# Kernel tuning notes

Measured on AMD Instinct MI355X. Metric: run time of the kernel, lower is better.

## Reference

```python
import jax, jax.numpy as jnp
import numpy as np

NEG = -1e9
CLIP = 10.0  # tanh clipping constant for SingleHeadAttention logits


def layer_norm(x, g, b, eps=1e-5):
    mu = jnp.mean(x, axis=-1, keepdims=True)
    var = jnp.var(x, axis=-1, keepdims=True)
    return (x - mu) * jax.lax.rsqrt(var + eps) * g + b


def setup_inputs() -> dict:
    key = jax.random.key(0)
    ks = jax.random.split(key, 16)
    B, A, N, E, Hf = 4096, 16, 128, 128, 128
    s = 0.02
    inp = {
        "agent_embed": jax.random.normal(ks[0], (B, A, E), jnp.float32),
        "city_embed": jax.random.normal(ks[1], (B, N, E), jnp.float32),
        "acts": jax.random.randint(ks[2], (B, A), 0, N, jnp.int32),
        # cross-attention layer params
        "Wq": jax.random.normal(ks[3], (E, E), jnp.float32) * s,
        "Wk": jax.random.normal(ks[4], (E, E), jnp.float32) * s,
        "Wv": jax.random.normal(ks[5], (E, E), jnp.float32) * s,
        "Wo": jax.random.normal(ks[6], (E, E), jnp.float32) * s,
        "ln1_g": jnp.ones((E,), jnp.float32),
        "ln1_b": jnp.zeros((E,), jnp.float32),
        "W1": jax.random.normal(ks[7], (E, Hf), jnp.float32) * s,
        "b1": jnp.zeros((Hf,), jnp.float32),
        "W2": jax.random.normal(ks[8], (Hf, E), jnp.float32) * s,
        "b2": jnp.zeros((E,), jnp.float32),
        "ln2_g": jnp.ones((E,), jnp.float32),
        "ln2_b": jnp.zeros((E,), jnp.float32),
        # single-head attention params
        "Wq_s": jax.random.normal(ks[9], (E, E), jnp.float32) * s,
        "Wk_s": jax.random.normal(ks[10], (E, E), jnp.float32) * s,
    }
    return inp


def reference(agent_embed, city_embed, acts, Wq, Wk, Wv, Wo, ln1_g, ln1_b,
              W1, b1, W2, b2, ln2_g, ln2_b, Wq_s, Wk_s):
    B, A, E = agent_embed.shape
    H = 8
    dh = E // H

    # ---- conflict mask construction ----
    eq = acts[:, :, None] == acts[:, None, :]            # [B,A,A] True = same city
    ident = jnp.eye(A, dtype=bool)[None]                 # [1,A,A]
    conflict = jnp.where(acts[:, :, None] == 0, ident, eq)
    mask = ~conflict                                     # True = blocked in attention

    # ---- gather per-agent selected city embeddings ----
    selected = jnp.take_along_axis(city_embed, acts[:, :, None].astype(jnp.int32), axis=1)  # [B,A,E]

    # ---- cross-attention layer (num_layers = 1) ----
    cac = selected
    q = (cac @ Wq).reshape(B, A, H, dh)
    k = (agent_embed @ Wk).reshape(B, A, H, dh)
    v = (agent_embed @ Wv).reshape(B, A, H, dh)
    scores = jnp.einsum("bqhd,bkhd->bhqk", q, k) / np.sqrt(dh).astype(np.float32)
    scores = jnp.where(mask[:, None, :, :], NEG, scores)
    attn = jax.nn.softmax(scores, axis=-1)
    out = jnp.einsum("bhqk,bkhd->bqhd", attn, v).reshape(B, A, E) @ Wo
    h = layer_norm(cac + out, ln1_g, ln1_b)
    ffn = jax.nn.relu(h @ W1 + b1) @ W2 + b2
    cac = layer_norm(h + ffn, ln2_g, ln2_b)

    # ---- single-head attention producing logits [B,A,A] ----
    qs = cac @ Wq_s
    ks_ = agent_embed @ Wk_s
    logits = jnp.einsum("bqe,bke->bqk", qs, ks_) / np.sqrt(E).astype(np.float32)
    logits = CLIP * jnp.tanh(logits)
    logits = jnp.where(mask, NEG, logits)
    return logits
```

## Files before the change

### kernel.cpp

```cpp
#include <hip/hip_runtime.h>
#include <hip/hip_bf16.h>
#include <math.h>

typedef __attribute__((ext_vector_type(8))) short bfrag;
typedef __attribute__((ext_vector_type(4))) short short4v;
typedef __attribute__((ext_vector_type(4))) float f32x4;

#define LDK 136

static __device__ __forceinline__ float b2f(short s)
{
    unsigned int u = ((unsigned int)(unsigned short)s) << 16;
    float f;
    __builtin_memcpy(&f, &u, 4);
    return f;
}

static __device__ __forceinline__ short4v pack4(f32x4 a)
{
    short4v o;
#pragma unroll
    for (int r = 0; r < 4; ++r) {
        __hip_bfloat16 h = __float2bfloat16(a[r]);
        short s;
        __builtin_memcpy(&s, &h, 2);
        o[r] = s;
    }
    return o;
}

static __device__ __forceinline__ bfrag pack8(f32x4 a, f32x4 b)
{
    bfrag o;
#pragma unroll
    for (int j = 0; j < 4; ++j) {
        __hip_bfloat16 h = __float2bfloat16(a[j]);
        short s;
        __builtin_memcpy(&s, &h, 2);
        o[j] = s;
    }
#pragma unroll
    for (int j = 0; j < 4; ++j) {
        __hip_bfloat16 h = __float2bfloat16(b[j]);
        short s;
        __builtin_memcpy(&s, &h, 2);
        o[4 + j] = s;
    }
    return o;
}

__global__ __launch_bounds__(256) void prep_weights(
    const float* __restrict__ Wq, const float* __restrict__ Wk,
    const float* __restrict__ Wv, const float* __restrict__ Wo,
    const float* __restrict__ W1, const float* __restrict__ W2,
    const float* __restrict__ Wqs, const float* __restrict__ Wks,
    __hip_bfloat16* __restrict__ out)
{
    __shared__ __hip_bfloat16 t[128 * 17];
    const float* Ws[8] = {Wq, Wk, Wv, Wo, W1, W2, Wqs, Wks};
    const int mat = blockIdx.x >> 3;
    const int slab = blockIdx.x & 7;
    const float* W = Ws[mat];
    const int n0 = slab * 16;

#pragma unroll
    for (int p = 0; p < 2; ++p) {
        int idx = p * 256 + threadIdx.x;
        int k = idx >> 2, c4 = idx & 3;
        float4 f = *(const float4*)(W + k * 128 + n0 + c4 * 4);
        __hip_bfloat16* d = t + k * 17 + c4 * 4;
        d[0] = __float2bfloat16(f.x); d[1] = __float2bfloat16(f.y);
        d[2] = __float2bfloat16(f.z); d[3] = __float2bfloat16(f.w);
    }
    __syncthreads();
    {
        int m = threadIdx.x >> 4;
        int idx = threadIdx.x & 15;
        int k0 = idx * 8;
        int kk = idx >> 2;
        int quad = idx & 3;
        __hip_bfloat16 v[8];
#pragma unroll
        for (int j = 0; j < 8; ++j) v[j] = t[(k0 + j) * 17 + m];
        __hip_bfloat16* o = out + (size_t)mat * 16384
                          + (size_t)(slab * 4 + kk) * 512 + (quad * 16 + m) * 8;
        *(bfrag*)o = *(const bfrag*)v;
    }
}

__device__ __forceinline__ void mmT8(const bfrag x[4],
                                     const __hip_bfloat16* sW,
                                     int lane, f32x4 acc[8])
{
    const f32x4 z = {0.f, 0.f, 0.f, 0.f};
#pragma unroll
    for (int ct = 0; ct < 8; ++ct) acc[ct] = z;
#pragma unroll
    for (int kk = 0; kk < 4; ++kk)
#pragma unroll
        for (int ct = 0; ct < 8; ++ct) {
            bfrag w = *(const bfrag*)(sW + (ct * 4 + kk) * 512 + lane * 8);
            acc[ct] = __builtin_amdgcn_mfma_f32_16x16x32_bf16(w, x[kk], acc[ct], 0, 0, 0);
        }
}

__device__ __forceinline__ void mmR8(const bfrag x[4],
                                     const __hip_bfloat16* sW,
                                     int lane, f32x4 acc[8])
{
    const f32x4 z = {0.f, 0.f, 0.f, 0.f};
#pragma unroll
    for (int ct = 0; ct < 8; ++ct) acc[ct] = z;
#pragma unroll
    for (int kk = 0; kk < 4; ++kk)
#pragma unroll
        for (int ct = 0; ct < 8; ++ct) {
            bfrag w = *(const bfrag*)(sW + (ct * 4 + kk) * 512 + lane * 8);
            acc[ct] = __builtin_amdgcn_mfma_f32_16x16x32_bf16(x[kk], w, acc[ct], 0, 0, 0);
        }
}

__global__ __launch_bounds__(256) void fused_model(
    const float* __restrict__ agent_embed,
    const float* __restrict__ city_embed,
    const int* __restrict__ acts,
    const __hip_bfloat16* __restrict__ wts,
    const float* __restrict__ ln1g, const float* __restrict__ ln1b,
    const float* __restrict__ b1, const float* __restrict__ b2,
    const float* __restrict__ ln2g, const float* __restrict__ ln2b,
    float* __restrict__ out)
{
    __shared__ __align__(16) __hip_bfloat16 sW[16384];
    __shared__ __align__(16) __hip_bfloat16 sbAll[4 * 16 * LDK];

    const int tid = threadIdx.x;
    const int wave = tid >> 6;
    const int lane = tid & 63;
    const int m = lane & 15;
    const int quad = lane >> 4;
    const int b = blockIdx.x * 4 + wave;
    __hip_bfloat16* const sb = sbAll + wave * (16 * LDK);

    bfrag wreg[8];

#define PRE(mat)                                                                \
    {                                                                           \
        const __hip_bfloat16* src = wts + (size_t)(mat) * 16384;                \
        _Pragma("unroll")                                                       \
        for (int i = 0; i < 8; ++i)                                             \
            wreg[i] = *(const bfrag*)(src + (i * 256 + tid) * 8);               \
    }
#define COMMIT()                                                                \
    {                                                                           \
        _Pragma("unroll")                                                       \
        for (int i = 0; i < 8; ++i)                                             \
            *(bfrag*)(sW + (i * 256 + tid) * 8) = wreg[i];                      \
    }

    const int aq = acts[b * 16 + m];
    bool keep[4];
#pragma unroll
    for (int r = 0; r < 4; ++r) {
        int ak = __shfl(aq, quad * 4 + r, 16);
        keep[r] = (aq == 0) ? (quad * 4 + r == m) : (ak == aq);
    }

    PRE(1);

    const float* arow = agent_embed + ((size_t)b * 16 + m) * 128;
    const float* crow = city_embed + ((size_t)b * 128 + aq) * 128;
    bfrag xa[4], xsk[4];
#pragma unroll
    for (int kk = 0; kk < 4; ++kk) {
        f32x4 a0 = *(const f32x4*)(arow + kk * 32 + quad * 8);
        f32x4 a1 = *(const f32x4*)(arow + kk * 32 + quad * 8 + 4);
        xa[kk] = pack8(a0, a1);
        f32x4 c0 = *(const f32x4*)(crow + kk * 32 + quad * 8);
        f32x4 c1 = *(const f32x4*)(crow + kk * 32 + quad * 8 + 4);
        xsk[kk] = pack8(c0, c1);
    }

    COMMIT();
    __syncthreads();

    f32x4 acc[8];
    short4v kf[8], vf[8], ksf[8], qf[8];

    PRE(2);
    mmT8(xa, sW, lane, acc);
#pragma unroll
    for (int ct = 0; ct < 8; ++ct) kf[ct] = pack4(acc[ct]);
    __syncthreads();
    COMMIT(); __syncthreads();

    PRE(7);
    mmR8(xa, sW, lane, acc);
#pragma unroll
    for (int ct = 0; ct < 8; ++ct) vf[ct] = pack4(acc[ct]);
    __syncthreads();
    COMMIT(); __syncthreads();

    PRE(0);
    mmT8(xa, sW, lane, acc);
#pragma unroll
    for (int ct = 0; ct < 8; ++ct) ksf[ct] = pack4(acc[ct]);
    __syncthreads();
    COMMIT(); __syncthreads();

    PRE(3);
    mmT8(xsk, sW, lane, acc);
#pragma unroll
    for (int ct = 0; ct < 8; ++ct) qf[ct] = pack4(acc[ct]);

    {
        const f32x4 z4 = {0.f, 0.f, 0.f, 0.f};
#pragma unroll
        for (int h = 0; h < 8; ++h) {
            f32x4 sc = __builtin_amdgcn_mfma_f32_16x16x16bf16_1k(kf[h], qf[h], z4, 0, 0, 0);
            float e[4], s = 0.f;
#pragma unroll
            for (int r = 0; r < 4; ++r) {
                e[r] = keep[r] ? __expf(sc[r] * 0.25f) : 0.f;
                s += e[r];
            }
            s += __shfl_xor(s, 16, 64);
            s += __shfl_xor(s, 32, 64);
            float inv = __builtin_amdgcn_rcpf(s);
            f32x4 p;
#pragma unroll
            for (int r = 0; r < 4; ++r) p[r] = e[r] * inv;
            short4v pa = pack4(p);
            f32x4 o4 = __builtin_amdgcn_mfma_f32_16x16x16bf16_1k(vf[h], pa, z4, 0, 0, 0);
            *(short4v*)(sb + m * LDK + h * 16 + quad * 4) = pack4(o4);
        }
    }
    bfrag xo[4];
#pragma unroll
    for (int kk = 0; kk < 4; ++kk)
        xo[kk] = *(const bfrag*)(sb + m * LDK + kk * 32 + quad * 8);
    __syncthreads();
    COMMIT(); __syncthreads();

    PRE(4);
    mmT8(xo, sW, lane, acc);
#pragma unroll
    for (int ct = 0; ct < 8; ++ct) {
        f32x4 cres = *(const f32x4*)(crow + ct * 16 + quad * 4);
#pragma unroll
        for (int r = 0; r < 4; ++r) acc[ct][r] += cres[r];
    }

    short4v hf[8];
    {
        float s = 0.f, s2 = 0.f;
#pragma unroll
        for (int ct = 0; ct < 8; ++ct)
#pragma unroll
            for (int r = 0; r < 4; ++r) { float v = acc[ct][r]; s += v; s2 += v * v; }
        s += __shfl_xor(s, 16, 64);  s += __shfl_xor(s, 32, 64);
        s2 += __shfl_xor(s2, 16, 64); s2 += __shfl_xor(s2, 32, 64);
        float mu = s * (1.f / 128.f);
        float var = s2 * (1.f / 128.f) - mu * mu;
        float rs = rsqrtf(var + 1e-5f);
#pragma unroll
        for (int ct = 0; ct < 8; ++ct) {
            f32x4 g4 = *(const f32x4*)(ln1g + ct * 16 + quad * 4);
            f32x4 bb4 = *(const f32x4*)(ln1b + ct * 16 + quad * 4);
            f32x4 hh;
#pragma unroll
            for (int r = 0; r < 4; ++r) hh[r] = (acc[ct][r] - mu) * rs * g4[r] + bb4[r];
            hf[ct] = pack4(hh);
            *(short4v*)(sb + m * LDK + ct * 16 + quad * 4) = hf[ct];
        }
    }
    bfrag hx[4];
#pragma unroll
    for (int kk = 0; kk < 4; ++kk)
        hx[kk] = *(const bfrag*)(sb + m * LDK + kk * 32 + quad * 8);
    __syncthreads();
    COMMIT(); __syncthreads();

    PRE(5);
    mmT8(hx, sW, lane, acc);
#pragma unroll
    for (int ct = 0; ct < 8; ++ct) {
        f32x4 bb4 = *(const f32x4*)(b1 + ct * 16 + quad * 4);
        f32x4 f;
#pragma unroll
        for (int r = 0; r < 4; ++r) f[r] = fmaxf(acc[ct][r] + bb4[r], 0.f);
        *(short4v*)(sb + m * LDK + ct * 16 + quad * 4) = pack4(f);
    }
    bfrag fx[4];
#pragma unroll
    for (int kk = 0; kk < 4; ++kk)
        fx[kk] = *(const bfrag*)(sb + m * LDK + kk * 32 + quad * 8);
    __syncthreads();
    COMMIT(); __syncthreads();

    PRE(6);
    mmT8(fx, sW, lane, acc);
#pragma unroll
    for (int ct = 0; ct < 8; ++ct) {
        f32x4 bb4 = *(const f32x4*)(b2 + ct * 16 + quad * 4);
#pragma unroll
        for (int r = 0; r < 4; ++r) acc[ct][r] += bb4[r] + b2f(hf[ct][r]);
    }

    {
        float s = 0.f, s2 = 0.f;
#pragma unroll
        for (int ct = 0; ct < 8; ++ct)
#pragma unroll
            for (int r = 0; r < 4; ++r) { float v = acc[ct][r]; s += v; s2 += v * v; }
        s += __shfl_xor(s, 16, 64);  s += __shfl_xor(s, 32, 64);
        s2 += __shfl_xor(s2, 16, 64); s2 += __shfl_xor(s2, 32, 64);
        float mu = s * (1.f / 128.f);
        float var = s2 * (1.f / 128.f) - mu * mu;
        float rs = rsqrtf(var + 1e-5f);
#pragma unroll
        for (int ct = 0; ct < 8; ++ct) {
            f32x4 g4 = *(const f32x4*)(ln2g + ct * 16 + quad * 4);
            f32x4 bb4 = *(const f32x4*)(ln2b + ct * 16 + quad * 4);
            f32x4 cc;
#pragma unroll
            for (int r = 0; r < 4; ++r) cc[r] = (acc[ct][r] - mu) * rs * g4[r] + bb4[r];
            *(short4v*)(sb + m * LDK + ct * 16 + quad * 4) = pack4(cc);
        }
    }
    bfrag cx[4];
#pragma unroll
    for (int kk = 0; kk < 4; ++kk)
        cx[kk] = *(const bfrag*)(sb + m * LDK + kk * 32 + quad * 8);
    __syncthreads();
    COMMIT(); __syncthreads();

    mmT8(cx, sW, lane, acc);

    {
        f32x4 la = {0.f, 0.f, 0.f, 0.f};
#pragma unroll
        for (int ct = 0; ct < 8; ++ct) {
            short4v qs4 = pack4(acc[ct]);
            la = __builtin_amdgcn_mfma_f32_16x16x16bf16_1k(ksf[ct], qs4, la, 0, 0, 0);
        }
        f32x4 o4;
#pragma unroll
        for (int r = 0; r < 4; ++r) {
            float v = la[r] * 0.0883883476483184f;
            v = 10.f * tanhf(v);
            o4[r] = keep[r] ? v : -1e9f;
        }
        *(f32x4*)(out + ((size_t)b * 16 + m) * 16 + quad * 4) = o4;
    }
#undef PRE
#undef COMMIT
}

extern "C" void kernel_launch(void* const* d_in, const int* in_sizes, int n_in,
                              void* d_out, int out_size, void* d_ws, size_t ws_size,
                              hipStream_t stream)
{
    const float* agent = (const float*)d_in[0];
    const float* city  = (const float*)d_in[1];
    const int*   acts  = (const int*)d_in[2];
    const float* Wq  = (const float*)d_in[3];
    const float* Wk  = (const float*)d_in[4];
    const float* Wv  = (const float*)d_in[5];
    const float* Wo  = (const float*)d_in[6];
    const float* l1g = (const float*)d_in[7];
    const float* l1b = (const float*)d_in[8];
    const float* W1  = (const float*)d_in[9];
    const float* b1  = (const float*)d_in[10];
    const float* W2  = (const float*)d_in[11];
    const float* b2  = (const float*)d_in[12];
    const float* l2g = (const float*)d_in[13];
    const float* l2b = (const float*)d_in[14];
    const float* Wqs = (const float*)d_in[15];
    const float* Wks = (const float*)d_in[16];
    float* out = (float*)d_out;

    int B = in_sizes[2] / 16;
    __hip_bfloat16* wts = (__hip_bfloat16*)d_ws;

    prep_weights<<<64, 256, 0, stream>>>(Wq, Wk, Wv, Wo, W1, W2, Wqs, Wks, wts);
    fused_model<<<B / 4, 256, 0, stream>>>(agent, city, acts, wts, l1g, l1b,
                                           b1, b2, l2g, l2b, out);
}
```

Before: 397.1 us.

## Process two batch problems per wave to reuse staged weight tiles

Each wave now handles two batch elements, so every weight fragment read from LDS feeds two MFMAs, and the grid is halved. This halves the per-problem weight staging, barrier and LDS-read overhead, and gives each wave two independent MFMA chains to interleave. In exchange it roughly doubles register pressure (launch bounds now request 2 blocks per SM), which may cause spills or lower occupancy, and it also doubles the per-block LDS scratch.

```diff
diff --git a/kernel.cpp b/kernel.cpp
--- a/kernel.cpp
+++ b/kernel.cpp
@@ -88,39 +88,41 @@
     }
 }
 
-__device__ __forceinline__ void mmT8(const bfrag x[4],
-                                     const __hip_bfloat16* sW,
-                                     int lane, f32x4 acc[8])
+__device__ __forceinline__ void mmT8x2(const bfrag x0[4], const bfrag x1[4],
+                                       const __hip_bfloat16* sW, int lane,
+                                       f32x4 acc0[8], f32x4 acc1[8])
 {
     const f32x4 z = {0.f, 0.f, 0.f, 0.f};
 #pragma unroll
-    for (int ct = 0; ct < 8; ++ct) acc[ct] = z;
+    for (int ct = 0; ct < 8; ++ct) { acc0[ct] = z; acc1[ct] = z; }
 #pragma unroll
     for (int kk = 0; kk < 4; ++kk)
 #pragma unroll
         for (int ct = 0; ct < 8; ++ct) {
             bfrag w = *(const bfrag*)(sW + (ct * 4 + kk) * 512 + lane * 8);
-            acc[ct] = __builtin_amdgcn_mfma_f32_16x16x32_bf16(w, x[kk], acc[ct], 0, 0, 0);
-        }
-}
-
-__device__ __forceinline__ void mmR8(const bfrag x[4],
-                                     const __hip_bfloat16* sW,
-                                     int lane, f32x4 acc[8])
+            acc0[ct] = __builtin_amdgcn_mfma_f32_16x16x32_bf16(w, x0[kk], acc0[ct], 0, 0, 0);
+            acc1[ct] = __builtin_amdgcn_mfma_f32_16x16x32_bf16(w, x1[kk], acc1[ct], 0, 0, 0);
+        }
+}
+
+__device__ __forceinline__ void mmR8x2(const bfrag x0[4], const bfrag x1[4],
+                                       const __hip_bfloat16* sW, int lane,
+                                       f32x4 acc0[8], f32x4 acc1[8])
 {
     const f32x4 z = {0.f, 0.f, 0.f, 0.f};
 #pragma unroll
-    for (int ct = 0; ct < 8; ++ct) acc[ct] = z;
+    for (int ct = 0; ct < 8; ++ct) { acc0[ct] = z; acc1[ct] = z; }
 #pragma unroll
     for (int kk = 0; kk < 4; ++kk)
 #pragma unroll
         for (int ct = 0; ct < 8; ++ct) {
             bfrag w = *(const bfrag*)(sW + (ct * 4 + kk) * 512 + lane * 8);
-            acc[ct] = __builtin_amdgcn_mfma_f32_16x16x32_bf16(x[kk], w, acc[ct], 0, 0, 0);
-        }
-}
-
-__global__ __launch_bounds__(256) void fused_model(
+            acc0[ct] = __builtin_amdgcn_mfma_f32_16x16x32_bf16(x0[kk], w, acc0[ct], 0, 0, 0);
+            acc1[ct] = __builtin_amdgcn_mfma_f32_16x16x32_bf16(x1[kk], w, acc1[ct], 0, 0, 0);
+        }
+}
+
+__global__ __launch_bounds__(256, 2) void fused_model(
     const float* __restrict__ agent_embed,
     const float* __restrict__ city_embed,
     const int* __restrict__ acts,
@@ -131,15 +133,17 @@
     float* __restrict__ out)
 {
     __shared__ __align__(16) __hip_bfloat16 sW[16384];
-    __shared__ __align__(16) __hip_bfloat16 sbAll[4 * 16 * LDK];
+    __shared__ __align__(16) __hip_bfloat16 sbAll[4 * 32 * LDK];
 
     const int tid = threadIdx.x;
     const int wave = tid >> 6;
     const int lane = tid & 63;
     const int m = lane & 15;
     const int quad = lane >> 4;
-    const int b = blockIdx.x * 4 + wave;
-    __hip_bfloat16* const sb = sbAll + wave * (16 * LDK);
+    const int p0 = blockIdx.x * 8 + wave * 2;
+    const int p1 = p0 + 1;
+    __hip_bfloat16* const sb0 = sbAll + wave * (32 * LDK);
+    __hip_bfloat16* const sb1 = sb0 + 16 * LDK;
 
     bfrag wreg[8];
 
@@ -157,200 +161,262 @@
             *(bfrag*)(sW + (i * 256 + tid) * 8) = wreg[i];                      \
     }
 
-    const int aq = acts[b * 16 + m];
-    bool keep[4];
+    const int aq0 = acts[p0 * 16 + m];
+    const int aq1 = acts[p1 * 16 + m];
+    bool keep0[4], keep1[4];
 #pragma unroll
     for (int r = 0; r < 4; ++r) {
-        int ak = __shfl(aq, quad * 4 + r, 16);
-        keep[r] = (aq == 0) ? (quad * 4 + r == m) : (ak == aq);
+        int ak0 = __shfl(aq0, quad * 4 + r, 16);
+        int ak1 = __shfl(aq1, quad * 4 + r, 16);
+        keep0[r] = (aq0 == 0) ? (quad * 4 + r == m) : (ak0 == aq0);
+        keep1[r] = (aq1 == 0) ? (quad * 4 + r == m) : (ak1 == aq1);
     }
 
     PRE(1);
 
-    const float* arow = agent_embed + ((size_t)b * 16 + m) * 128;
-    const float* crow = city_embed + ((size_t)b * 128 + aq) * 128;
-    bfrag xa[4], xsk[4];
+    const float* arow0 = agent_embed + ((size_t)p0 * 16 + m) * 128;
+    const float* arow1 = agent_embed + ((size_t)p1 * 16 + m) * 128;
+    const float* crow0 = city_embed + ((size_t)p0 * 128 + aq0) * 128;
+    const float* crow1 = city_embed + ((size_t)p1 * 128 + aq1) * 128;
+    bfrag xa0[4], xa1[4], xsk0[4], xsk1[4];
 #pragma unroll
     for (int kk = 0; kk < 4; ++kk) {
-        f32x4 a0 = *(const f32x4*)(arow + kk * 32 + quad * 8);
-        f32x4 a1 = *(const f32x4*)(arow + kk * 32 + quad * 8 + 4);
-        xa[kk] = pack8(a0, a1);
-        f32x4 c0 = *(const f32x4*)(crow + kk * 32 + quad * 8);
-        f32x4 c1 = *(const f32x4*)(crow + kk * 32 + quad * 8 + 4);
-        xsk[kk] = pack8(c0, c1);
+        xa0[kk] = pack8(*(const f32x4*)(arow0 + kk * 32 + quad * 8),
+                        *(const f32x4*)(arow0 + kk * 32 + quad * 8 + 4));
+        xa1[kk] = pack8(*(const f32x4*)(arow1 + kk * 32 + quad * 8),
+                        *(const f32x4*)(arow1 + kk * 32 + quad * 8 + 4));
+        xsk0[kk] = pack8(*(const f32x4*)(crow0 + kk * 32 + quad * 8),
+                         *(const f32x4*)(crow0 + kk * 32 + quad * 8 + 4));
+        xsk1[kk] = pack8(*(const f32x4*)(crow1 + kk * 32 + quad * 8),
+                         *(const f32x4*)(crow1 + kk * 32 + quad * 8 + 4));
     }
 
     COMMIT();
     __syncthreads();
 
-    f32x4 acc[8];
-    short4v kf[8], vf[8], ksf[8], qf[8];
+    f32x4 acc0[8], acc1[8];
+    short4v kf0[8], kf1[8], vf0[8], vf1[8], ksf0[8], ksf1[8], qf0[8], qf1[8];
 
     PRE(2);
-    mmT8(xa, sW, lane, acc);
-#pragma unroll
-    for (int ct = 0; ct < 8; ++ct) kf[ct] = pack4(acc[ct]);
+    mmT8x2(xa0, xa1, sW, lane, acc0, acc1);
+#pragma unroll
+    for (int ct = 0; ct < 8; ++ct) { kf0[ct] = pack4(acc0[ct]); kf1[ct] = pack4(acc1[ct]); }
     __syncthreads();
     COMMIT(); __syncthreads();
 
     PRE(7);
-    mmR8(xa, sW, lane, acc);
-#pragma unroll
-    for (int ct = 0; ct < 8; ++ct) vf[ct] = pack4(acc[ct]);
+    mmR8x2(xa0, xa1, sW, lane, acc0, acc1);
+#pragma unroll
+    for (int ct = 0; ct < 8; ++ct) { vf0[ct] = pack4(acc0[ct]); vf1[ct] = pack4(acc1[ct]); }
     __syncthreads();
     COMMIT(); __syncthreads();
 
     PRE(0);
-    mmT8(xa, sW, lane, acc);
-#pragma unroll
-    for (int ct = 0; ct < 8; ++ct) ksf[ct] = pack4(acc[ct]);
+    mmT8x2(xa0, xa1, sW, lane, acc0, acc1);
+#pragma unroll
+    for (int ct = 0; ct < 8; ++ct) { ksf0[ct] = pack4(acc0[ct]); ksf1[ct] = pack4(acc1[ct]); }
     __syncthreads();
     COMMIT(); __syncthreads();
 
     PRE(3);
-    mmT8(xsk, sW, lane, acc);
-#pragma unroll
-    for (int ct = 0; ct < 8; ++ct) qf[ct] = pack4(acc[ct]);
+    mmT8x2(xsk0, xsk1, sW, lane, acc0, acc1);
+#pragma unroll
+    for (int ct = 0; ct < 8; ++ct) { qf0[ct] = pack4(acc0[ct]); qf1[ct] = pack4(acc1[ct]); }
 
     {
         const f32x4 z4 = {0.f, 0.f, 0.f, 0.f};
 #pragma unroll
         for (int h = 0; h < 8; ++h) {
-            f32x4 sc = __builtin_amdgcn_mfma_f32_16x16x16bf16_1k(kf[h], qf[h], z4, 0, 0, 0);
-            float e[4], s = 0.f;
+            {
+                f32x4 sc = __builtin_amdgcn_mfma_f32_16x16x16bf16_1k(kf0[h], qf0[h], z4, 0, 0, 0);
+                float e[4], s = 0.f;
+#pragma unroll
+                for (int r = 0; r < 4; ++r) {
+                    e[r] = keep0[r] ? __expf(sc[r] * 0.25f) : 0.f;
+                    s += e[r];
+                }
+                s += __shfl_xor(s, 16, 64);
+                s += __shfl_xor(s, 32, 64);
+                float inv = __builtin_amdgcn_rcpf(s);
+                f32x4 p;
+#pragma unroll
+                for (int r = 0; r < 4; ++r) p[r] = e[r] * inv;
+                f32x4 o4 = __builtin_amdgcn_mfma_f32_16x16x16bf16_1k(vf0[h], pack4(p), z4, 0, 0, 0);
+                *(short4v*)(sb0 + m * LDK + h * 16 + quad * 4) = pack4(o4);
+            }
+            {
+                f32x4 sc = __builtin_amdgcn_mfma_f32_16x16x16bf16_1k(kf1[h], qf1[h], z4, 0, 0, 0);
+                float e[4], s = 0.f;
+#pragma unroll
+                for (int r = 0; r < 4; ++r) {
+                    e[r] = keep1[r] ? __expf(sc[r] * 0.25f) : 0.f;
+                    s += e[r];
+                }
+                s += __shfl_xor(s, 16, 64);
+                s += __shfl_xor(s, 32, 64);
+                float inv = __builtin_amdgcn_rcpf(s);
+                f32x4 p;
+#pragma unroll
+                for (int r = 0; r < 4; ++r) p[r] = e[r] * inv;
+                f32x4 o4 = __builtin_amdgcn_mfma_f32_16x16x16bf16_1k(vf1[h], pack4(p), z4, 0, 0, 0);
+                *(short4v*)(sb1 + m * LDK + h * 16 + quad * 4) = pack4(o4);
+            }
+        }
+    }
+    bfrag xo0[4], xo1[4];
+#pragma unroll
+    for (int kk = 0; kk < 4; ++kk) {
+        xo0[kk] = *(const bfrag*)(sb0 + m * LDK + kk * 32 + quad * 8);
+        xo1[kk] = *(const bfrag*)(sb1 + m * LDK + kk * 32 + quad * 8);
+    }
+    __syncthreads();
+    COMMIT(); __syncthreads();
+
+    PRE(4);
+    mmT8x2(xo0, xo1, sW, lane, acc0, acc1);
+#pragma unroll
+    for (int ct = 0; ct < 8; ++ct) {
+        f32x4 c0 = *(const f32x4*)(crow0 + ct * 16 + quad * 4);
+        f32x4 c1 = *(const f32x4*)(crow1 + ct * 16 + quad * 4);
+#pragma unroll
+        for (int r = 0; r < 4; ++r) { acc0[ct][r] += c0[r]; acc1[ct][r] += c1[r]; }
+    }
+
+    short4v hf0[8], hf1[8];
+    {
+        float s0 = 0.f, s20 = 0.f, s1 = 0.f, s21 = 0.f;
+#pragma unroll
+        for (int ct = 0; ct < 8; ++ct)
 #pragma unroll
             for (int r = 0; r < 4; ++r) {
-                e[r] = keep[r] ? __expf(sc[r] * 0.25f) : 0.f;
-                s += e[r];
-            }
-            s += __shfl_xor(s, 16, 64);
-            s += __shfl_xor(s, 32, 64);
-            float inv = __builtin_amdgcn_rcpf(s);
-            f32x4 p;
-#pragma unroll
-            for (int r = 0; r < 4; ++r) p[r] = e[r] * inv;
-            short4v pa = pack4(p);
-            f32x4 o4 = __builtin_amdgcn_mfma_f32_16x16x16bf16_1k(vf[h], pa, z4, 0, 0, 0);
-            *(short4v*)(sb + m * LDK + h * 16 + quad * 4) = pack4(o4);
-        }
-    }
-    bfrag xo[4];
-#pragma unroll
-    for (int kk = 0; kk < 4; ++kk)
-        xo[kk] = *(const bfrag*)(sb + m * LDK + kk * 32 + quad * 8);
-    __syncthreads();
-    COMMIT(); __syncthreads();
-
-    PRE(4);
-    mmT8(xo, sW, lane, acc);
-#pragma unroll
-    for (int ct = 0; ct < 8; ++ct) {
-        f32x4 cres = *(const f32x4*)(crow + ct * 16 + quad * 4);
-#pragma unroll
-        for (int r = 0; r < 4; ++r) acc[ct][r] += cres[r];
-    }
-
-    short4v hf[8];
-    {
-        float s = 0.f, s2 = 0.f;
-#pragma unroll
-        for (int ct = 0; ct < 8; ++ct)
-#pragma unroll
-            for (int r = 0; r < 4; ++r) { float v = acc[ct][r]; s += v; s2 += v * v; }
-        s += __shfl_xor(s, 16, 64);  s += __shfl_xor(s, 32, 64);
-        s2 += __shfl_xor(s2, 16, 64); s2 += __shfl_xor(s2, 32, 64);
-        float mu = s * (1.f / 128.f);
-        float var = s2 * (1.f / 128.f) - mu * mu;
-        float rs = rsqrtf(var + 1e-5f);
+                float v0 = acc0[ct][r]; s0 += v0; s20 += v0 * v0;
+                float v1 = acc1[ct][r]; s1 += v1; s21 += v1 * v1;
+            }
+        s0 += __shfl_xor(s0, 16, 64);  s0 += __shfl_xor(s0, 32, 64);
+        s20 += __shfl_xor(s20, 16, 64); s20 += __shfl_xor(s20, 32, 64);
+        s1 += __shfl_xor(s1, 16, 64);  s1 += __shfl_xor(s1, 32, 64);
+        s21 += __shfl_xor(s21, 16, 64); s21 += __shfl_xor(s21, 32, 64);
+        float mu0 = s0 * (1.f / 128.f), mu1 = s1 * (1.f / 128.f);
+        float rs0 = rsqrtf(s20 * (1.f / 128.f) - mu0 * mu0 + 1e-5f);
+        float rs1 = rsqrtf(s21 * (1.f / 128.f) - mu1 * mu1 + 1e-5f);
 #pragma unroll
         for (int ct = 0; ct < 8; ++ct) {
             f32x4 g4 = *(const f32x4*)(ln1g + ct * 16 + quad * 4);
             f32x4 bb4 = *(const f32x4*)(ln1b + ct * 16 + quad * 4);
-            f32x4 hh;
-#pragma unroll
-            for (int r = 0; r < 4; ++r) hh[r] = (acc[ct][r] - mu) * rs * g4[r] + bb4[r];
-            hf[ct] = pack4(hh);
-            *(short4v*)(sb + m * LDK + ct * 16 + quad * 4) = hf[ct];
-        }
-    }
-    bfrag hx[4];
-#pragma unroll
-    for (int kk = 0; kk < 4; ++kk)
-        hx[kk] = *(const bfrag*)(sb + m * LDK + kk * 32 + quad * 8);
+            f32x4 h0, h1;
+#pragma unroll
+            for (int r = 0; r < 4; ++r) {
+                h0[r] = (acc0[ct][r] - mu0) * rs0 * g4[r] + bb4[r];
+                h1[r] = (acc1[ct][r] - mu1) * rs1 * g4[r] + bb4[r];
+            }
+            hf0[ct] = pack4(h0); hf1[ct] = pack4(h1);
+            *(short4v*)(sb0 + m * LDK + ct * 16 + quad * 4) = hf0[ct];
+            *(short4v*)(sb1 + m * LDK + ct * 16 + quad * 4) = hf1[ct];
+        }
+    }
+    bfrag hx0[4], hx1[4];
+#pragma unroll
+    for (int kk = 0; kk < 4; ++kk) {
+        hx0[kk] = *(const bfrag*)(sb0 + m * LDK + kk * 32 + quad * 8);
+        hx1[kk] = *(const bfrag*)(sb1 + m * LDK + kk * 32 + quad * 8);
+    }
     __syncthreads();
     COMMIT(); __syncthreads();
 
     PRE(5);
-    mmT8(hx, sW, lane, acc);
+    mmT8x2(hx0, hx1, sW, lane, acc0, acc1);
 #pragma unroll
     for (int ct = 0; ct < 8; ++ct) {
         f32x4 bb4 = *(const f32x4*)(b1 + ct * 16 + quad * 4);
-        f32x4 f;
-#pragma unroll
-        for (int r = 0; r < 4; ++r) f[r] = fmaxf(acc[ct][r] + bb4[r], 0.f);
-        *(short4v*)(sb + m * LDK + ct * 16 + quad * 4) = pack4(f);
-    }
-    bfrag fx[4];
-#pragma unroll
-    for (int kk = 0; kk < 4; ++kk)
-        fx[kk] = *(const bfrag*)(sb + m * LDK + kk * 32 + quad * 8);
+        f32x4 f0, f1;
+#pragma unroll
+        for (int r = 0; r < 4; ++r) {
+            f0[r] = fmaxf(acc0[ct][r] + bb4[r], 0.f);
+            f1[r] = fmaxf(acc1[ct][r] + bb4[r], 0.f);
+        }
+        *(short4v*)(sb0 + m * LDK + ct * 16 + quad * 4) = pack4(f0);
+        *(short4v*)(sb1 + m * LDK + ct * 16 + quad * 4) = pack4(f1);
+    }
+    bfrag fx0[4], fx1[4];
+#pragma unroll
+    for (int kk = 0; kk < 4; ++kk) {
+        fx0[kk] = *(const bfrag*)(sb0 + m * LDK + kk * 32 + quad * 8);
+        fx1[kk] = *(const bfrag*)(sb1 + m * LDK + kk * 32 + quad * 8);
+    }
     __syncthreads();
     COMMIT(); __syncthreads();
 
     PRE(6);
-    mmT8(fx, sW, lane, acc);
+    mmT8x2(fx0, fx1, sW, lane, acc0, acc1);
 #pragma unroll
     for (int ct = 0; ct < 8; ++ct) {
         f32x4 bb4 = *(const f32x4*)(b2 + ct * 16 + quad * 4);
 #pragma unroll
-        for (int r = 0; r < 4; ++r) acc[ct][r] += bb4[r] + b2f(hf[ct][r]);
+        for (int r = 0; r < 4; ++r) {
+            acc0[ct][r] += bb4[r] + b2f(hf0[ct][r]);
+            acc1[ct][r] += bb4[r] + b2f(hf1[ct][r]);
+        }
     }
 
     {
-        float s = 0.f, s2 = 0.f;
+        float s0 = 0.f, s20 = 0.f, s1 = 0.f, s21 = 0.f;
 #pragma unroll
         for (int ct = 0; ct < 8; ++ct)
 #pragma unroll
-            for (int r = 0; r < 4; ++r) { float v = acc[ct][r]; s += v; s2 += v * v; }
-        s += __shfl_xor(s, 16, 64);  s += __shfl_xor(s, 32, 64);
-        s2 += __shfl_xor(s2, 16, 64); s2 += __shfl_xor(s2, 32, 64);
-        float mu = s * (1.f / 128.f);
-        float var = s2 * (1.f / 128.f) - mu * mu;
-        float rs = rsqrtf(var + 1e-5f);
+            for (int r = 0; r < 4; ++r) {
+                float v0 = acc0[ct][r]; s0 += v0; s20 += v0 * v0;
+                float v1 = acc1[ct][r]; s1 += v1; s21 += v1 * v1;
+            }
+        s0 += __shfl_xor(s0, 16, 64);  s0 += __shfl_xor(s0, 32, 64);
+        s20 += __shfl_xor(s20, 16, 64); s20 += __shfl_xor(s20, 32, 64);
+        s1 += __shfl_xor(s1, 16, 64);  s1 += __shfl_xor(s1, 32, 64);
+        s21 += __shfl_xor(s21, 16, 64); s21 += __shfl_xor(s21, 32, 64);
+        float mu0 = s0 * (1.f / 128.f), mu1 = s1 * (1.f / 128.f);
+        float rs0 = rsqrtf(s20 * (1.f / 128.f) - mu0 * mu0 + 1e-5f);
+        float rs1 = rsqrtf(s21 * (1.f / 128.f) - mu1 * mu1 + 1e-5f);
 #pragma unroll
         for (int ct = 0; ct < 8; ++ct) {
             f32x4 g4 = *(const f32x4*)(ln2g + ct * 16 + quad * 4);
             f32x4 bb4 = *(const f32x4*)(ln2b + ct * 16 + quad * 4);
-            f32x4 cc;
-#pragma unroll
-            for (int r = 0; r < 4; ++r) cc[r] = (acc[ct][r] - mu) * rs * g4[r] + bb4[r];
-            *(short4v*)(sb + m * LDK + ct * 16 + quad * 4) = pack4(cc);
-        }
-    }
-    bfrag cx[4];
-#pragma unroll
-    for (int kk = 0; kk < 4; ++kk)
-        cx[kk] = *(const bfrag*)(sb + m * LDK + kk * 32 + quad * 8);
-    __syncthreads();
-    COMMIT(); __syncthreads();
-
-    mmT8(cx, sW, lane, acc);
+            f32x4 c0, c1;
+#pragma unroll
+            for (int r = 0; r < 4; ++r) {
+                c0[r] = (acc0[ct][r] - mu0) * rs0 * g4[r] + bb4[r];
+                c1[r] = (acc1[ct][r] - mu1) * rs1 * g4[r] + bb4[r];
+            }
+            *(short4v*)(sb0 + m * LDK + ct * 16 + quad * 4) = pack4(c0);
+            *(short4v*)(sb1 + m * LDK + ct * 16 + quad * 4) = pack4(c1);
+        }
+    }
+    bfrag cx0[4], cx1[4];
+#pragma unroll
+    for (int kk = 0; kk < 4; ++kk) {
+        cx0[kk] = *(const bfrag*)(sb0 + m * LDK + kk * 32 + quad * 8);
+        cx1[kk] = *(const bfrag*)(sb1 + m * LDK + kk * 32 + quad * 8);
+    }
+    __syncthreads();
+    COMMIT(); __syncthreads();
+
+    mmT8x2(cx0, cx1, sW, lane, acc0, acc1);
 
     {
-        f32x4 la = {0.f, 0.f, 0.f, 0.f};
+        f32x4 la0 = {0.f, 0.f, 0.f, 0.f};
+        f32x4 la1 = {0.f, 0.f, 0.f, 0.f};
 #pragma unroll
         for (int ct = 0; ct < 8; ++ct) {
-            short4v qs4 = pack4(acc[ct]);
-            la = __builtin_amdgcn_mfma_f32_16x16x16bf16_1k(ksf[ct], qs4, la, 0, 0, 0);
-        }
-        f32x4 o4;
+            la0 = __builtin_amdgcn_mfma_f32_16x16x16bf16_1k(ksf0[ct], pack4(acc0[ct]), la0, 0, 0, 0);
+            la1 = __builtin_amdgcn_mfma_f32_16x16x16bf16_1k(ksf1[ct], pack4(acc1[ct]), la1, 0, 0, 0);
+        }
+        f32x4 o0, o1;
 #pragma unroll
         for (int r = 0; r < 4; ++r) {
-            float v = la[r] * 0.0883883476483184f;
-            v = 10.f * tanhf(v);
-            o4[r] = keep[r] ? v : -1e9f;
-        }
-        *(f32x4*)(out + ((size_t)b * 16 + m) * 16 + quad * 4) = o4;
+            float v0 = 10.f * tanhf(la0[r] * 0.0883883476483184f);
+            float v1 = 10.f * tanhf(la1[r] * 0.0883883476483184f);
+            o0[r] = keep0[r] ? v0 : -1e9f;
+            o1[r] = keep1[r] ? v1 : -1e9f;
+        }
+        *(f32x4*)(out + ((size_t)p0 * 16 + m) * 16 + quad * 4) = o0;
+        *(f32x4*)(out + ((size_t)p1 * 16 + m) * 16 + quad * 4) = o1;
     }
 #undef PRE
 #undef COMMIT
@@ -383,6 +449,6 @@
     __hip_bfloat16* wts = (__hip_bfloat16*)d_ws;
 
     prep_weights<<<64, 256, 0, stream>>>(Wq, Wk, Wv, Wo, W1, W2, Wqs, Wks, wts);
-    fused_model<<<B / 4, 256, 0, stream>>>(agent, city, acts, wts, l1g, l1b,
+    fused_model<<<B / 8, 256, 0, stream>>>(agent, city, acts, wts, l1g, l1b,
                                            b1, b2, l2g, l2b, out);
 }
```

Result: faster. 382.8 us (-3.6%).
